# Performance work log

Hardware: AMD Instinct MI355X
Metric: run time of the kernel (lower is better)

Reference implementation:

```python
import jax, jax.numpy as jnp
import numpy as np

V = 64                 # |Sigma|
IN_DIM = V + 2         # Sigma + '(' + ')'
OUT_DIM = V + 1        # Sigma + <del>/<end>
H = 512
B = 256
SX = 34                # max proto length 32 + 2 boundaries
SY = 34
BIG_NEG = -1000000000.0


def _one_hot_seq(key, S, batch):
    # '(' at pos 0, L random symbols, ')' at pos L+1, zero padding after
    kl, ks = jax.random.split(key)
    lengths = jax.random.randint(kl, (batch,), 4, S - 1)        # L in [4, S-2]
    syms = jax.random.randint(ks, (S, batch), 0, V)
    pos = jnp.arange(S)[:, None]
    tok = jnp.where(pos == 0, V, jnp.where(pos == lengths[None, :] + 1, V + 1, syms))
    oh = jax.nn.one_hot(tok, IN_DIM, dtype=jnp.float32)
    valid = (pos <= lengths[None, :] + 1).astype(jnp.float32)
    return oh * valid[:, :, None]


def setup_inputs() -> dict:
    key = jax.random.key(0)
    ks = jax.random.split(key, 14)

    def p(k, shape, scale):
        return jax.random.uniform(k, shape, jnp.float32, -scale, scale)

    s = 1.0 / float(np.sqrt(H))
    s2 = 1.0 / float(np.sqrt(2 * H))
    return {
        "sources": _one_hot_seq(ks[0], SX, B),
        "targets": _one_hot_seq(ks[1], SY, B),
        # bidirectional prior LSTM (input IN_DIM -> hidden H, fwd + rev)
        "Wih_f": p(ks[2], (4 * H, IN_DIM), s), "Whh_f": p(ks[3], (4 * H, H), s), "b_f": p(ks[4], (4 * H,), s),
        "Wih_r": p(ks[5], (4 * H, IN_DIM), s), "Whh_r": p(ks[6], (4 * H, H), s), "b_r": p(ks[7], (4 * H,), s),
        # modern LSTM (input IN_DIM -> hidden 2H)
        "Wih_m": p(ks[8], (8 * H, IN_DIM), s2), "Whh_m": p(ks[9], (8 * H, 2 * H), s2), "b_m": p(ks[10], (8 * H,), s2),
        # heads: Linear(2H -> OUT_DIM) + LogSoftmax
        "W_sub": p(ks[11], (OUT_DIM, 2 * H), s2), "b_sub": jnp.zeros((OUT_DIM,), jnp.float32),
        "W_ins": p(ks[12], (OUT_DIM, 2 * H), s2), "b_ins": jnp.zeros((OUT_DIM,), jnp.float32),
    }


def _lstm(x, Wih, Whh, b, hid):
    # torch gate order: i, f, g, o
    bsz = x.shape[1]
    def step(carry, xt):
        h, c = carry
        g = xt @ Wih.T + h @ Whh.T + b
        i, f, gg, o = jnp.split(g, 4, axis=-1)
        c = jax.nn.sigmoid(f) * c + jax.nn.sigmoid(i) * jnp.tanh(gg)
        h = jax.nn.sigmoid(o) * jnp.tanh(c)
        return (h, c), h
    init = (jnp.zeros((bsz, hid), x.dtype), jnp.zeros((bsz, hid), x.dtype))
    _, hs = jax.lax.scan(step, init, x)
    return hs  # [S, B, hid]


def _forward(sources, targets, Wih_f, Whh_f, b_f, Wih_r, Whh_r, b_r,
             Wih_m, Whh_m, b_m, W_sub, b_sub, W_ins, b_ins):
    x_fwd = _lstm(sources, Wih_f, Whh_f, b_f, H)
    x_bwd = _lstm(sources[::-1], Wih_r, Whh_r, b_r, H)[::-1]
    x_emb = jnp.concatenate([x_fwd, x_bwd], axis=-1)   # [SX, B, 2H]
    y_emb = _lstm(targets, Wih_m, Whh_m, b_m, 2 * H)    # [SY, B, 2H]

    # head(x_emb[i] + y_emb[j]) decomposes since Linear is affine
    def pair_logprobs(W, bb):
        lx = jnp.einsum('ibh,oh->ibo', x_emb, W)              # [SX, B, O]
        ly = jnp.einsum('jbh,oh->jbo', y_emb, W) + bb         # [SY, B, O]
        return jax.nn.log_softmax(lx[:, None] + ly[None, :], axis=-1)  # [SX, SY, B, O]

    sub_log = pair_logprobs(W_sub, b_sub)
    ins_log = pair_logprobs(W_ins, b_ins)

    # cell (i, j, b) is computed iff x[i] and y[j] are real (non-padding) one-hots, j <= max_cognat_length
    x_any = sources.sum(-1) > 0                                # [SX, B]
    y_any = targets.sum(-1) > 0                                # [SY, B]
    j_ok = jnp.arange(SY) < SY - 1
    valid = x_any[:, None, :] & (y_any & j_ok[:, None])[None, :, :]   # [SX, SY, B]

    end = jnp.where(valid, ins_log[..., V], BIG_NEG)           # insProbs[V_SIZE]
    dlt = jnp.where(valid, sub_log[..., V], BIG_NEG)           # subProbs[V_SIZE]

    y_next = jnp.pad(targets[1:], ((0, 1), (0, 0), (0, 0)))    # y[j+1], [SY, B, IN_DIM]
    ins_ok = valid & (y_next[..., IN_DIM - 1] == 0)[None]      # not bool(y[j+1, V_SIZE+1])
    ins_val = jnp.einsum('ijbv,jbv->ijb', ins_log[..., :V], y_next[..., :V])
    sub_val = jnp.einsum('ijbv,jbv->ijb', sub_log[..., :V], y_next[..., :V])

    # stacked cached probs: [ins, sub, end, del], each [SX, SY, B]
    return jnp.stack([
        jnp.where(ins_ok, ins_val, BIG_NEG),
        jnp.where(ins_ok, sub_val, BIG_NEG),
        end,
        dlt,
    ])


def reference(sources, targets, Wih_f, Whh_f, b_f, Wih_r, Whh_r, b_r,
              Wih_m, Whh_m, b_m, W_sub, b_sub, W_ins, b_ins):
    return _forward(sources, targets, Wih_f, Whh_f, b_f, Wih_r, Whh_r, b_r,
                    Wih_m, Whh_m, b_m, W_sub, b_sub, W_ins, b_ins)
```

## Files before the change

### kernel.cpp

```cpp
#include <hip/hip_runtime.h>

typedef __attribute__((ext_vector_type(4))) float f32x4;
typedef unsigned char u8;
typedef unsigned long long u64t;

#define BIG_NEG -1000000000.0f

static constexpr int B_  = 256;
static constexpr int SX_ = 34;
static constexpr int SY_ = 34;
static constexpr int IND = 66;
static constexpr int OP_ = 80;

__device__ __forceinline__ f32x4 mfma_fp8(long a, long b, f32x4 c) {
  return __builtin_amdgcn_mfma_f32_16x16x32_fp8_fp8(a, b, c, 0, 0, 0);
}
__device__ __forceinline__ float sigm(float x)  { return 1.0f / (1.0f + __expf(-x)); }
__device__ __forceinline__ float tanhx(float x) { return 2.0f * sigm(2.0f * x) - 1.0f; }
template <bool HI>
__device__ __forceinline__ unsigned pk2(float a, float b, unsigned old) {
  return __builtin_amdgcn_cvt_pk_fp8_f32(a, b, (int)old, HI);
}

__global__ __launch_bounds__(256) void prep_all(
    const float* __restrict__ src, const float* __restrict__ tgt,
    int* __restrict__ tok_x, int* __restrict__ tok_y,
    const float* __restrict__ Wsub, const float* __restrict__ Wins,
    u8* __restrict__ Wcat,
    const float* __restrict__ Wihf, const float* __restrict__ bf,
    const float* __restrict__ Wihr, const float* __restrict__ br,
    const float* __restrict__ Wihm, const float* __restrict__ bm,
    float* __restrict__ Ef, float* __restrict__ Er, float* __restrict__ Em,
    const float* __restrict__ Whf, const float* __restrict__ Whr,
    const float* __restrict__ Whm,
    u8* __restrict__ w8f, u8* __restrict__ w8r, u8* __restrict__ w8m) {
  __shared__ float tile[64 * 67];
  const int blk = blockIdx.x;
  const int tid = threadIdx.x;

  if (blk < 68) {
    int idx = blk * 256 + tid;
    const int half = SX_ * B_;
    const float* base = (idx < half) ? src : tgt;
    int* outp         = (idx < half) ? tok_x : tok_y;
    int k = (idx < half) ? idx : idx - half;
    const float* p = base + (size_t)k * IND;
    int tok = -1;
    for (int v = 0; v < IND; ++v) if (p[v] > 0.5f) tok = v;
    outp[k] = tok;
  } else if (blk < 228) {
    int widx = (blk - 68) * 256 + tid;
    int row = widx >> 8;
    int wc  = widx & 255;
    int srow = row < 80 ? row : row - 80;
    const float* W = row < 80 ? Wsub : Wins;
    float f0 = 0.f, f1 = 0.f, f2 = 0.f, f3 = 0.f;
    if (srow < 65) {
      const float* p = W + (size_t)srow * 1024 + wc * 4;
      f0 = p[0]; f1 = p[1]; f2 = p[2]; f3 = p[3];
    }
    unsigned w = pk2<false>(f0, f1, 0);
    w = pk2<true>(f2, f3, w);
    ((unsigned*)Wcat)[widx] = w;
  } else if (blk < 356) {
    int tb = blk - 228;
    const float* W; const float* bias; float* E; int H4; int n0;
    if (tb < 32)      { W = Wihf; bias = bf; E = Ef; H4 = 2048; n0 = tb * 64; }
    else if (tb < 64) { W = Wihr; bias = br; E = Er; H4 = 2048; n0 = (tb - 32) * 64; }
    else              { W = Wihm; bias = bm; E = Em; H4 = 4096; n0 = (tb - 64) * 64; }
    const float* s2 = W + (size_t)n0 * IND;
    for (int i = tid; i < 64 * IND; i += 256) {
      int n = i / IND, v = i - n * IND;
      tile[n * 67 + v] = s2[i];
    }
    __syncthreads();
    int lane = tid & 63, w2 = tid >> 6;
    float bl = bias[n0 + lane];
    for (int v = w2; v < 67; v += 4) {
      float val = (v < 66 ? tile[lane * 67 + v] : 0.f) + bl;
      E[(size_t)v * H4 + n0 + lane] = val;
    }
  } else {
    const int F4 = 2048 * 512 / 4;
    const int M4 = 4096 * 1024 / 4;
    int i = (blk - 356) * 256 + tid;
    int stride = 3072 * 256;
    for (; i < 2 * F4 + M4; i += stride) {
      const float* s3; unsigned* dst; int k;
      if (i < F4)          { s3 = Whf; dst = (unsigned*)w8f; k = i; }
      else if (i < 2 * F4) { s3 = Whr; dst = (unsigned*)w8r; k = i - F4; }
      else                 { s3 = Whm; dst = (unsigned*)w8m; k = i - 2 * F4; }
      float4 f = ((const float4*)s3)[k];
      unsigned w3 = pk2<false>(f.x, f.y, 0);
      w3 = pk2<true>(f.z, f.w, w3);
      dst[k] = w3;
    }
  }
}

template <int HH, int NS>
__device__ __forceinline__ void run_lstm(
    const u8* __restrict__ w8, const float* __restrict__ E,
    bool revr, u8* __restrict__ hall, int b0, int h0,
    unsigned* __restrict__ flags, int dom0, int myid,
    u8* __restrict__ alds, u8* __restrict__ hT, const u8* __restrict__ tok_small) {
  const int tid = threadIdx.x;
  const int lane = tid & 63, w = tid >> 6;
  const int lo = lane & 15, q = lane >> 4;
  constexpr int AST = HH + 8;
  constexpr int U8C = HH / 8;
  constexpr int USH = (HH == 1024) ? 7 : 6;
  constexpr int NI  = (32 * U8C) / 256;
  constexpr int NK  = HH / 32;
  const int hh = lo & 7;
  const bool hi = (lo >= 8);
  const int hu_e = h0 + w * 8 + hh;

  long breg0[NK], breg1[NK];
  {
    const u8* brow0 = w8 + (size_t)((lo >> 3) * HH + hu_e) * HH + q * 8;
    const u8* brow1 = w8 + (size_t)((2 + (lo >> 3)) * HH + hu_e) * HH + q * 8;
#pragma unroll
    for (int kk = 0; kk < NK; ++kk) {
      breg0[kk] = *(const long*)(brow0 + kk * 32);
      breg1[kk] = *(const long*)(brow1 + kk * 32);
    }
  }
  float creg[4] = {0.f, 0.f, 0.f, 0.f};

  for (int t = 0; t < 34; ++t) {
    f32x4 acc[2][2];
#pragma unroll
    for (int mt = 0; mt < 2; ++mt) {
      acc[mt][0] = (f32x4){0.f, 0.f, 0.f, 0.f};
      acc[mt][1] = (f32x4){0.f, 0.f, 0.f, 0.f};
    }

    if (t > 0) {
      const u8* hsrc = hall + (size_t)t * (256 * HH);
      u64t tmp[NI];
#pragma unroll
      for (int ii = 0; ii < NI; ++ii) {
        int idx = tid + ii * 256;
        tmp[ii] = __hip_atomic_load(
            (const u64t*)(hsrc + (size_t)(b0 + (idx >> USH)) * HH + (idx & (U8C - 1)) * 8),
            __ATOMIC_RELAXED, __HIP_MEMORY_SCOPE_AGENT);
      }
#pragma unroll
      for (int ii = 0; ii < NI; ++ii) {
        int idx = tid + ii * 256;
        *(u64t*)&alds[(idx >> USH) * AST + (idx & (U8C - 1)) * 8] = tmp[ii];
      }
      __syncthreads();

      const u8* a0p = alds + lo * AST + q * 8;
      const u8* a1p = alds + (16 + lo) * AST + q * 8;
#pragma unroll
      for (int kk = 0; kk < NK; ++kk) {
        long a0 = *(const long*)(a0p + kk * 32);
        long a1 = *(const long*)(a1p + kk * 32);
        acc[0][0] = mfma_fp8(a0, breg0[kk], acc[0][0]);
        acc[0][1] = mfma_fp8(a0, breg1[kk], acc[0][1]);
        acc[1][0] = mfma_fp8(a1, breg0[kk], acc[1][0]);
        acc[1][1] = mfma_fp8(a1, breg1[kk], acc[1][1]);
      }
    }

    int tpos = revr ? 33 - t : t;
    const u8* tkp = tok_small + tpos * 32;
#pragma unroll
    for (int mt = 0; mt < 2; ++mt) {
      f32x4 t0 = acc[mt][0], t1 = acc[mt][1];
      f32x4 p0, p1;
#pragma unroll
      for (int c2 = 0; c2 < 4; ++c2) {
        p0[c2] = __shfl_xor(t0[c2], 8, 64);
        p1[c2] = __shfl_xor(t1[c2], 8, 64);
      }
#pragma unroll
      for (int rr = 0; rr < 2; ++rr) {
        int r = (hi ? 2 : 0) + rr;
        float iv = hi ? p0[r] : t0[r];
        float fv = hi ? t0[r] : p0[r];
        float gv = hi ? p1[r] : t1[r];
        float ov = hi ? t1[r] : p1[r];
        int m = mt * 16 + q * 4 + r;
        int v = tkp[m];
        const float* e = E + (size_t)v * (4 * HH) + hu_e;
        iv += e[0]; fv += e[HH]; gv += e[2 * HH]; ov += e[3 * HH];
        float cold = creg[mt * 2 + rr];
        float cn = sigm(fv) * cold + sigm(iv) * tanhx(gv);
        float hn = sigm(ov) * tanhx(cn);
        creg[mt * 2 + rr] = cn;
        hT[m * 32 + w * 8 + hh] = (u8)(pk2<false>(hn, hn, 0) & 0xffu);
      }
    }
    __syncthreads();

    {
      int m = tid >> 3, cc = tid & 7;
      unsigned val = *(const unsigned*)&hT[m * 32 + cc * 4];
      u8* hdst = hall + (size_t)(t + 1) * (256 * HH);
      __hip_atomic_store((unsigned*)(hdst + (size_t)(b0 + m) * HH + h0 + cc * 4),
                         val, __ATOMIC_RELAXED, __HIP_MEMORY_SCOPE_AGENT);
    }

    if (t < 33) {
      __asm__ volatile("s_waitcnt vmcnt(0)" ::: "memory");
      __syncthreads();
      unsigned tgt = (unsigned)(t + 1);
      if (tid == 0)
        __hip_atomic_store(&flags[(dom0 + myid) * 32], tgt,
                           __ATOMIC_RELAXED, __HIP_MEMORY_SCOPE_AGENT);
      if (tid < NS) {
        int spin = 0;
        for (;;) {
          unsigned v = __hip_atomic_load(&flags[(dom0 + tid) * 32],
                                         __ATOMIC_RELAXED, __HIP_MEMORY_SCOPE_AGENT);
          if (__ballot(v < tgt) == 0) break;
          __builtin_amdgcn_s_sleep(1);
          if (++spin > (1 << 17)) break;
        }
      }
      __syncthreads();
    }
  }
}

__global__ __launch_bounds__(256, 2) void lstm_persist(
    const int* __restrict__ tok_x, const int* __restrict__ tok_y,
    const float* __restrict__ E_f, const u8* __restrict__ w8_f,
    const float* __restrict__ E_r, const u8* __restrict__ w8_r,
    const float* __restrict__ E_m, const u8* __restrict__ w8_m,
    u8* __restrict__ fwd_all, u8* __restrict__ rev_all, u8* __restrict__ y_all,
    unsigned* __restrict__ flags) {
  __shared__ u8 alds[32 * 1032];
  __shared__ u8 hT[32 * 32];
  __shared__ u8 tok_small[34 * 32];

  const int b = blockIdx.x;
  int role, c, s;
  if (b < 256)      { role = 2; c = b >> 5; s = b & 31; }
  else if (b < 384) { int l = b - 256; role = 0; c = l >> 4; s = l & 15; }
  else              { int l = b - 384; role = 1; c = l >> 4; s = l & 15; }

  const float* E  = role == 0 ? E_f  : role == 1 ? E_r  : E_m;
  const u8*    w8 = role == 0 ? w8_f : role == 1 ? w8_r : w8_m;
  u8* hall        = role == 0 ? fwd_all : role == 1 ? rev_all : y_all;
  const int* tokg = (role == 2) ? tok_y : tok_x;
  const int b0 = c * 32;
  const int h0 = s * 32;
  const int dom0 = (role == 2) ? c * 32 : (role == 0) ? 256 + c * 16 : 384 + c * 16;

  for (int i = threadIdx.x; i < 34 * 32; i += 256) {
    int t2 = i >> 5, m = i & 31;
    int tk = tokg[t2 * 256 + b0 + m];
    tok_small[i] = (u8)(tk < 0 ? 66 : tk);
  }
  __syncthreads();

  if (role == 2)
    run_lstm<1024, 32>(w8, E, false, hall, b0, h0, flags, dom0, s, alds, hT, tok_small);
  else
    run_lstm<512, 16>(w8, E, role == 1, hall, b0, h0, flags, dom0, s, alds, hT, tok_small);
}

__global__ __launch_bounds__(256, 1) void head_kernel(
    const u8* __restrict__ fwd_all, const u8* __restrict__ rev_all,
    const u8* __restrict__ y_all, const u8* __restrict__ Wcat,
    const float* __restrict__ b_sub, const float* __restrict__ b_ins,
    float* __restrict__ lx_sub, float* __restrict__ lx_ins,
    float* __restrict__ ly_sub, float* __restrict__ ly_ins) {
  __shared__ u8 wq[160 * 264];
  const int lane = threadIdx.x & 63, wave = threadIdx.x >> 6;
  const int lo = lane & 15, q = lane >> 4;
  int blk = blockIdx.x;
  bool yside = (blk >= 136);
  int mb = yside ? blk - 136 : blk;
  int ij = mb >> 2;
  int bbase = (mb & 3) * 64;

  f32x4 acc[10];
#pragma unroll
  for (int nn = 0; nn < 10; ++nn) acc[nn] = (f32x4){0.f,0.f,0.f,0.f};

  for (int qk = 0; qk < 4; ++qk) {
    long aA[8];
    {
      int row = bbase + wave * 16 + lo;
      const u8* ab;
      if (yside)
        ab = y_all + ((size_t)(ij + 1) * 256 + row) * 1024 + qk * 256 + q * 8;
      else if (qk < 2)
        ab = fwd_all + ((size_t)(ij + 1) * 256 + row) * 512 + qk * 256 + q * 8;
      else
        ab = rev_all + ((size_t)(34 - ij) * 256 + row) * 512 + (qk - 2) * 256 + q * 8;
#pragma unroll
      for (int ki = 0; ki < 8; ++ki) aA[ki] = *(const long*)(ab + ki * 32);
    }

    for (int c8 = threadIdx.x; c8 < 160 * 32; c8 += 256) {
      int row = c8 >> 5, col = (c8 & 31) << 3;
      *(long*)&wq[row * 264 + col] =
          *(const long*)&Wcat[(size_t)row * 1024 + qk * 256 + col];
    }
    __syncthreads();

#pragma unroll
    for (int ki = 0; ki < 8; ++ki) {
#pragma unroll
      for (int nn = 0; nn < 10; ++nn) {
        long bf = *(const long*)&wq[(nn * 16 + lo) * 264 + ki * 32 + q * 8];
        acc[nn] = mfma_fp8(aA[ki], bf, acc[nn]);
      }
    }
    __syncthreads();
  }

#pragma unroll
  for (int nn = 0; nn < 10; ++nn) {
    bool is_sub = (nn < 5);
    int n = (is_sub ? nn : nn - 5) * 16 + lo;
    float bias = 0.0f;
    if (yside && n < 65) bias = is_sub ? b_sub[n] : b_ins[n];
    float* dst = yside ? (is_sub ? ly_sub : ly_ins) : (is_sub ? lx_sub : lx_ins);
#pragma unroll
    for (int r = 0; r < 4; ++r) {
      int b = bbase + wave * 16 + q * 4 + r;
      dst[((size_t)ij * 256 + b) * OP_ + n] = acc[nn][r] + bias;
    }
  }
}

__device__ __forceinline__ void lse_one(const float4* __restrict__ X,
                                        const float* __restrict__ py, int sym,
                                        float& logZ, float& v64, float& vs) {
  float v[68];
  const float4* py4 = (const float4*)py;
#pragma unroll
  for (int q = 0; q < 17; ++q) {
    float4 yb = py4[q];
    v[4 * q + 0] = X[q].x + yb.x;
    v[4 * q + 1] = X[q].y + yb.y;
    v[4 * q + 2] = X[q].z + yb.z;
    v[4 * q + 3] = X[q].w + yb.w;
  }
  float m = v[0];
#pragma unroll
  for (int o = 1; o < 65; ++o) m = fmaxf(m, v[o]);
  float s = 0.0f, vsl = 0.0f;
#pragma unroll
  for (int o = 0; o < 65; ++o) {
    s += __expf(v[o] - m);
    if (o < 64) vsl = (o == sym) ? v[o] : vsl;
  }
  logZ = m + __logf(s);
  v64 = v[64];
  vs = vsl;
}

__global__ __launch_bounds__(256, 1) void pair_kernel(
    const int* __restrict__ tok_x, const int* __restrict__ tok_y,
    const float* __restrict__ lx_sub, const float* __restrict__ lx_ins,
    const float* __restrict__ ly_sub, const float* __restrict__ ly_ins,
    float* __restrict__ out) {
  const int hsel = blockIdx.x >= 136;
  const int rem = hsel ? blockIdx.x - 136 : blockIdx.x;
  const int i = rem >> 2;
  const int bc = rem & 3;
  const int jq = threadIdx.x >> 6;
  const int bl = threadIdx.x & 63;
  const int b = bc * 64 + bl;
  const size_t CH = (size_t)SX_ * SY_ * B_;
  const float* lx = hsel ? lx_ins : lx_sub;
  const float* ly = hsel ? ly_ins : ly_sub;
  float* outA = out + (hsel ? 0 : CH);
  float* outB = out + (hsel ? 2 * CH : 3 * CH);

  float4 X[17];
  {
    const float4* ps = (const float4*)(lx + ((size_t)i * 256 + b) * OP_);
#pragma unroll
    for (int q = 0; q < 17; ++q) X[q] = ps[q];
  }
  int tx = tok_x[i * 256 + b];

  for (int j = jq; j < 34; j += 4) {
    size_t obase = ((size_t)i * SY_ + j) * 256 + b;
    bool dead = (j == SY_ - 1) || (tx < 0);
    if (!dead) {
      int ty = tok_y[j * 256 + b];
      if (ty < 0) dead = true;
    }
    if (dead) {
      outA[obase] = BIG_NEG;
      outB[obase] = BIG_NEG;
      continue;
    }
    int tn = tok_y[(j + 1) * 256 + b];
    bool ins_ok = (tn != 65);
    int sym = (tn >= 0 && tn < 64) ? tn : -1;

    float logZ, v64, vs;
    lse_one(X, ly + ((size_t)j * 256 + b) * OP_, sym, logZ, v64, vs);
    float valB = v64 - logZ;
    float valA = (sym >= 0) ? (vs - logZ) : 0.0f;
    outA[obase] = ins_ok ? valA : BIG_NEG;
    outB[obase] = valB;
  }
}

extern "C" void kernel_launch(void* const* d_in, const int* in_sizes, int n_in,
                              void* d_out, int out_size, void* d_ws, size_t ws_size,
                              hipStream_t stream) {
  const float* sources = (const float*)d_in[0];
  const float* targets = (const float*)d_in[1];
  const float* Wih_f = (const float*)d_in[2];
  const float* Whh_f = (const float*)d_in[3];
  const float* b_f   = (const float*)d_in[4];
  const float* Wih_r = (const float*)d_in[5];
  const float* Whh_r = (const float*)d_in[6];
  const float* b_r   = (const float*)d_in[7];
  const float* Wih_m = (const float*)d_in[8];
  const float* Whh_m = (const float*)d_in[9];
  const float* b_m   = (const float*)d_in[10];
  const float* W_sub = (const float*)d_in[11];
  const float* b_sub = (const float*)d_in[12];
  const float* W_ins = (const float*)d_in[13];
  const float* b_ins = (const float*)d_in[14];
  float* out = (float*)d_out;

  char* w = (char*)d_ws;
  constexpr size_t FLAG_SZ = 512 * 32 * 4;
  constexpr size_t TOK_SZ  = (size_t)SX_ * B_ * 4;
  constexpr size_t WCAT_SZ = (size_t)160 * 1024;
  constexpr size_t W8F_SZ  = (size_t)2048 * 512;
  constexpr size_t W8M_SZ  = (size_t)4096 * 1024;
  constexpr size_t EF_SZ   = (size_t)67 * 2048 * 4;
  constexpr size_t EM_SZ   = (size_t)67 * 4096 * 4;
  constexpr size_t LX_SZ   = (size_t)SX_ * B_ * OP_ * 4;
  constexpr size_t HF_SZ   = (size_t)35 * B_ * 512;
  constexpr size_t HM_SZ   = (size_t)35 * B_ * 1024;

  size_t off = 0;
  unsigned* flags = (unsigned*)(w + off); off += FLAG_SZ;
  int*  tok_x   = (int*)(w + off);  off += TOK_SZ;
  int*  tok_y   = (int*)(w + off);  off += TOK_SZ;
  off = (off + 255) & ~(size_t)255;
  u8*   Wcat    = (u8*)(w + off);   off += WCAT_SZ;
  u8*   w8_f    = (u8*)(w + off);   off += W8F_SZ;
  u8*   w8_r    = (u8*)(w + off);   off += W8F_SZ;
  u8*   w8_m    = (u8*)(w + off);   off += W8M_SZ;
  float* E_f    = (float*)(w + off); off += EF_SZ;
  float* E_r    = (float*)(w + off); off += EF_SZ;
  float* E_m    = (float*)(w + off); off += EM_SZ;
  float* lx_sub = (float*)(w + off); off += LX_SZ;
  float* lx_ins = (float*)(w + off); off += LX_SZ;
  float* ly_sub = (float*)(w + off); off += LX_SZ;
  float* ly_ins = (float*)(w + off); off += LX_SZ;
  u8* fwd_all   = (u8*)(w + off);   off += HF_SZ;
  u8* rev_all   = (u8*)(w + off);   off += HF_SZ;
  u8* y_all     = (u8*)(w + off);   off += HM_SZ;
  (void)ws_size; (void)in_sizes; (void)n_in; (void)out_size;

  (void)hipMemsetAsync(flags, 0, FLAG_SZ, stream);

  prep_all<<<3428, 256, 0, stream>>>(
      sources, targets, tok_x, tok_y,
      W_sub, W_ins, Wcat,
      Wih_f, b_f, Wih_r, b_r, Wih_m, b_m, E_f, E_r, E_m,
      Whh_f, Whh_r, Whh_m, w8_f, w8_r, w8_m);

  lstm_persist<<<512, 256, 0, stream>>>(
      tok_x, tok_y,
      E_f, w8_f,
      E_r, w8_r,
      E_m, w8_m,
      fwd_all, rev_all, y_all, flags);

  head_kernel<<<272, 256, 0, stream>>>(fwd_all, rev_all, y_all, Wcat,
                                       b_sub, b_ins, lx_sub, lx_ins, ly_sub, ly_ins);

  pair_kernel<<<272, 256, 0, stream>>>(tok_x, tok_y, lx_sub, lx_ins,
                                       ly_sub, ly_ins, out);
}
```

Baseline: 338.6 us.

## Split LSTM batch tile into two half-tiles with separate flags to overlap sync

The persistent LSTM kernel now processes each 32-row batch tile as two 16-row halves, each with its own completion flag domain. The second half's hidden-state loads and input-embedding gathers are issued while the first half's results are published, and separate waves wait on each half's flags. The aim is to shorten the critical path of the per-timestep cross-block barrier by letting dependent blocks start on half A before half B is done. In exchange there are more __syncthreads per step, a larger flag array, and half-width MFMA work per phase.

```diff
diff --git a/kernel.cpp b/kernel.cpp
--- a/kernel.cpp
+++ b/kernel.cpp
@@ -98,11 +98,36 @@
   }
 }
 
+__device__ __forceinline__ void lstm_epi(
+    f32x4 t0, f32x4 t1, const float (&e)[4][2], float (&creg)[2],
+    int r0, bool hi, int q, int w, int hh, u8* __restrict__ hT) {
+  f32x4 p0, p1;
+#pragma unroll
+  for (int c2 = 0; c2 < 4; ++c2) {
+    p0[c2] = __shfl_xor(t0[c2], 8, 64);
+    p1[c2] = __shfl_xor(t1[c2], 8, 64);
+  }
+#pragma unroll
+  for (int rr = 0; rr < 2; ++rr) {
+    int r = r0 + rr;
+    float iv = (hi ? p0[r] : t0[r]) + e[0][rr];
+    float fv = (hi ? t0[r] : p0[r]) + e[1][rr];
+    float gv = (hi ? p1[r] : t1[r]) + e[2][rr];
+    float ov = (hi ? t1[r] : p1[r]) + e[3][rr];
+    int m = q * 4 + r;
+    float cold = creg[rr];
+    float cn = sigm(fv) * cold + sigm(iv) * tanhx(gv);
+    float hn = sigm(ov) * tanhx(cn);
+    creg[rr] = cn;
+    hT[m * 32 + w * 8 + hh] = (u8)(pk2<false>(hn, hn, 0) & 0xffu);
+  }
+}
+
 template <int HH, int NS>
-__device__ __forceinline__ void run_lstm(
+__device__ __forceinline__ void run_lstm2(
     const u8* __restrict__ w8, const float* __restrict__ E,
     bool revr, u8* __restrict__ hall, int b0, int h0,
-    unsigned* __restrict__ flags, int dom0, int myid,
+    unsigned* __restrict__ flags, int fA, int fB, int myid,
     u8* __restrict__ alds, u8* __restrict__ hT, const u8* __restrict__ tok_small) {
   const int tid = threadIdx.x;
   const int lane = tid & 63, w = tid >> 6;
@@ -110,11 +135,12 @@
   constexpr int AST = HH + 8;
   constexpr int U8C = HH / 8;
   constexpr int USH = (HH == 1024) ? 7 : 6;
-  constexpr int NI  = (32 * U8C) / 256;
+  constexpr int NI  = (16 * U8C) / 256;
   constexpr int NK  = HH / 32;
   const int hh = lo & 7;
   const bool hi = (lo >= 8);
   const int hu_e = h0 + w * 8 + hh;
+  const int r0 = hi ? 2 : 0;
 
   long breg0[NK], breg1[NK];
   {
@@ -126,104 +152,136 @@
       breg1[kk] = *(const long*)(brow1 + kk * 32);
     }
   }
-  float creg[4] = {0.f, 0.f, 0.f, 0.f};
+  float cregA[2] = {0.f, 0.f};
+  float cregB[2] = {0.f, 0.f};
 
   for (int t = 0; t < 34; ++t) {
-    f32x4 acc[2][2];
-#pragma unroll
-    for (int mt = 0; mt < 2; ++mt) {
-      acc[mt][0] = (f32x4){0.f, 0.f, 0.f, 0.f};
-      acc[mt][1] = (f32x4){0.f, 0.f, 0.f, 0.f};
-    }
-
+    const int tpos = revr ? 33 - t : t;
+    const u8* tk_base = tok_small + tpos * 32;
+    const u8* hsrc = hall + (size_t)t * (256 * HH);
+    u8* hdst = hall + (size_t)(t + 1) * (256 * HH);
+
+    float eA[4][2];
     if (t > 0) {
-      const u8* hsrc = hall + (size_t)t * (256 * HH);
-      u64t tmp[NI];
+      u64t tmpA[NI];
 #pragma unroll
       for (int ii = 0; ii < NI; ++ii) {
         int idx = tid + ii * 256;
-        tmp[ii] = __hip_atomic_load(
+        tmpA[ii] = __hip_atomic_load(
             (const u64t*)(hsrc + (size_t)(b0 + (idx >> USH)) * HH + (idx & (U8C - 1)) * 8),
             __ATOMIC_RELAXED, __HIP_MEMORY_SCOPE_AGENT);
       }
 #pragma unroll
+      for (int rr = 0; rr < 2; ++rr) {
+        int v = tk_base[q * 4 + r0 + rr];
+        const float* e = E + (size_t)v * (4 * HH) + hu_e;
+        eA[0][rr] = e[0]; eA[1][rr] = e[HH]; eA[2][rr] = e[2 * HH]; eA[3][rr] = e[3 * HH];
+      }
+#pragma unroll
       for (int ii = 0; ii < NI; ++ii) {
         int idx = tid + ii * 256;
-        *(u64t*)&alds[(idx >> USH) * AST + (idx & (U8C - 1)) * 8] = tmp[ii];
+        *(u64t*)&alds[(idx >> USH) * AST + (idx & (U8C - 1)) * 8] = tmpA[ii];
       }
       __syncthreads();
-
-      const u8* a0p = alds + lo * AST + q * 8;
-      const u8* a1p = alds + (16 + lo) * AST + q * 8;
+    } else {
+#pragma unroll
+      for (int rr = 0; rr < 2; ++rr) {
+        int v = tk_base[q * 4 + r0 + rr];
+        const float* e = E + (size_t)v * (4 * HH) + hu_e;
+        eA[0][rr] = e[0]; eA[1][rr] = e[HH]; eA[2][rr] = e[2 * HH]; eA[3][rr] = e[3 * HH];
+      }
+    }
+
+    f32x4 accA0 = (f32x4){0.f, 0.f, 0.f, 0.f};
+    f32x4 accA1 = (f32x4){0.f, 0.f, 0.f, 0.f};
+    if (t > 0) {
+      const u8* ap = alds + lo * AST + q * 8;
 #pragma unroll
       for (int kk = 0; kk < NK; ++kk) {
-        long a0 = *(const long*)(a0p + kk * 32);
-        long a1 = *(const long*)(a1p + kk * 32);
-        acc[0][0] = mfma_fp8(a0, breg0[kk], acc[0][0]);
-        acc[0][1] = mfma_fp8(a0, breg1[kk], acc[0][1]);
-        acc[1][0] = mfma_fp8(a1, breg0[kk], acc[1][0]);
-        acc[1][1] = mfma_fp8(a1, breg1[kk], acc[1][1]);
-      }
-    }
-
-    int tpos = revr ? 33 - t : t;
-    const u8* tkp = tok_small + tpos * 32;
-#pragma unroll
-    for (int mt = 0; mt < 2; ++mt) {
-      f32x4 t0 = acc[mt][0], t1 = acc[mt][1];
-      f32x4 p0, p1;
-#pragma unroll
-      for (int c2 = 0; c2 < 4; ++c2) {
-        p0[c2] = __shfl_xor(t0[c2], 8, 64);
-        p1[c2] = __shfl_xor(t1[c2], 8, 64);
-      }
-#pragma unroll
-      for (int rr = 0; rr < 2; ++rr) {
-        int r = (hi ? 2 : 0) + rr;
-        float iv = hi ? p0[r] : t0[r];
-        float fv = hi ? t0[r] : p0[r];
-        float gv = hi ? p1[r] : t1[r];
-        float ov = hi ? t1[r] : p1[r];
-        int m = mt * 16 + q * 4 + r;
-        int v = tkp[m];
-        const float* e = E + (size_t)v * (4 * HH) + hu_e;
-        iv += e[0]; fv += e[HH]; gv += e[2 * HH]; ov += e[3 * HH];
-        float cold = creg[mt * 2 + rr];
-        float cn = sigm(fv) * cold + sigm(iv) * tanhx(gv);
-        float hn = sigm(ov) * tanhx(cn);
-        creg[mt * 2 + rr] = cn;
-        hT[m * 32 + w * 8 + hh] = (u8)(pk2<false>(hn, hn, 0) & 0xffu);
-      }
-    }
-    __syncthreads();
-
-    {
-      int m = tid >> 3, cc = tid & 7;
-      unsigned val = *(const unsigned*)&hT[m * 32 + cc * 4];
-      u8* hdst = hall + (size_t)(t + 1) * (256 * HH);
-      __hip_atomic_store((unsigned*)(hdst + (size_t)(b0 + m) * HH + h0 + cc * 4),
+        long av = *(const long*)(ap + kk * 32);
+        accA0 = mfma_fp8(av, breg0[kk], accA0);
+        accA1 = mfma_fp8(av, breg1[kk], accA1);
+      }
+    }
+    lstm_epi(accA0, accA1, eA, cregA, r0, hi, q, w, hh, hT);
+    __syncthreads();
+
+    float eB[4][2];
+    u64t tmpB[NI];
+    if (t > 0) {
+#pragma unroll
+      for (int ii = 0; ii < NI; ++ii) {
+        int idx = tid + ii * 256;
+        tmpB[ii] = __hip_atomic_load(
+            (const u64t*)(hsrc + (size_t)(b0 + 16 + (idx >> USH)) * HH + (idx & (U8C - 1)) * 8),
+            __ATOMIC_RELAXED, __HIP_MEMORY_SCOPE_AGENT);
+      }
+    }
+    if (w == 0) {
+      int m = lane >> 2, c8 = lane & 3;
+      u64t val = *(const u64t*)&hT[m * 32 + c8 * 8];
+      __hip_atomic_store((u64t*)(hdst + (size_t)(b0 + m) * HH + h0 + c8 * 8),
                          val, __ATOMIC_RELAXED, __HIP_MEMORY_SCOPE_AGENT);
-    }
-
-    if (t < 33) {
       __asm__ volatile("s_waitcnt vmcnt(0)" ::: "memory");
-      __syncthreads();
-      unsigned tgt = (unsigned)(t + 1);
-      if (tid == 0)
-        __hip_atomic_store(&flags[(dom0 + myid) * 32], tgt,
+      if (lane == 0 && t < 33)
+        __hip_atomic_store(&flags[(fA + myid) * 32], (unsigned)(t + 1),
                            __ATOMIC_RELAXED, __HIP_MEMORY_SCOPE_AGENT);
-      if (tid < NS) {
+    }
+#pragma unroll
+    for (int rr = 0; rr < 2; ++rr) {
+      int v = tk_base[16 + q * 4 + r0 + rr];
+      const float* e = E + (size_t)v * (4 * HH) + hu_e;
+      eB[0][rr] = e[0]; eB[1][rr] = e[HH]; eB[2][rr] = e[2 * HH]; eB[3][rr] = e[3 * HH];
+    }
+    if (t > 0) {
+#pragma unroll
+      for (int ii = 0; ii < NI; ++ii) {
+        int idx = tid + ii * 256;
+        *(u64t*)&alds[(16 + (idx >> USH)) * AST + (idx & (U8C - 1)) * 8] = tmpB[ii];
+      }
+    }
+    __syncthreads();
+
+    f32x4 accB0 = (f32x4){0.f, 0.f, 0.f, 0.f};
+    f32x4 accB1 = (f32x4){0.f, 0.f, 0.f, 0.f};
+    if (t > 0) {
+      const u8* ap = alds + (16 + lo) * AST + q * 8;
+#pragma unroll
+      for (int kk = 0; kk < NK; ++kk) {
+        long av = *(const long*)(ap + kk * 32);
+        accB0 = mfma_fp8(av, breg0[kk], accB0);
+        accB1 = mfma_fp8(av, breg1[kk], accB1);
+      }
+    }
+    lstm_epi(accB0, accB1, eB, cregB, r0, hi, q, w, hh, hT);
+    __syncthreads();
+
+    if (w == 0) {
+      int m = lane >> 2, c8 = lane & 3;
+      u64t val = *(const u64t*)&hT[m * 32 + c8 * 8];
+      __hip_atomic_store((u64t*)(hdst + (size_t)(b0 + 16 + m) * HH + h0 + c8 * 8),
+                         val, __ATOMIC_RELAXED, __HIP_MEMORY_SCOPE_AGENT);
+      if (t < 33) {
+        __asm__ volatile("s_waitcnt vmcnt(0)" ::: "memory");
+        if (lane == 0)
+          __hip_atomic_store(&flags[(fB + myid) * 32], (unsigned)(t + 1),
+                             __ATOMIC_RELAXED, __HIP_MEMORY_SCOPE_AGENT);
+      }
+    } else if ((w == 2 || w == 3) && t < 33) {
+      const int base = (w == 2) ? fA : fB;
+      const unsigned tgt = (unsigned)(t + 1);
+      if (lane < NS) {
         int spin = 0;
         for (;;) {
-          unsigned v = __hip_atomic_load(&flags[(dom0 + tid) * 32],
+          unsigned v = __hip_atomic_load(&flags[(base + lane) * 32],
                                          __ATOMIC_RELAXED, __HIP_MEMORY_SCOPE_AGENT);
           if (__ballot(v < tgt) == 0) break;
           __builtin_amdgcn_s_sleep(1);
           if (++spin > (1 << 17)) break;
         }
       }
-      __syncthreads();
-    }
+    }
+    __syncthreads();
   }
 }
 
@@ -234,8 +292,8 @@
     const float* __restrict__ E_m, const u8* __restrict__ w8_m,
     u8* __restrict__ fwd_all, u8* __restrict__ rev_all, u8* __restrict__ y_all,
     unsigned* __restrict__ flags) {
-  __shared__ u8 alds[32 * 1032];
-  __shared__ u8 hT[32 * 32];
+  __shared__ u8 alds[32 * 1032] __attribute__((aligned(16)));
+  __shared__ u8 hT[16 * 32] __attribute__((aligned(16)));
   __shared__ u8 tok_small[34 * 32];
 
   const int b = blockIdx.x;
@@ -250,7 +308,10 @@
   const int* tokg = (role == 2) ? tok_y : tok_x;
   const int b0 = c * 32;
   const int h0 = s * 32;
-  const int dom0 = (role == 2) ? c * 32 : (role == 0) ? 256 + c * 16 : 384 + c * 16;
+  int fA, fB;
+  if (role == 2)      { fA = c * 64;        fB = fA + 32; }
+  else if (role == 0) { fA = 512 + c * 32;  fB = fA + 16; }
+  else                { fA = 768 + c * 32;  fB = fA + 16; }
 
   for (int i = threadIdx.x; i < 34 * 32; i += 256) {
     int t2 = i >> 5, m = i & 31;
@@ -260,9 +321,9 @@
   __syncthreads();
 
   if (role == 2)
-    run_lstm<1024, 32>(w8, E, false, hall, b0, h0, flags, dom0, s, alds, hT, tok_small);
+    run_lstm2<1024, 32>(w8, E, false, hall, b0, h0, flags, fA, fB, s, alds, hT, tok_small);
   else
-    run_lstm<512, 16>(w8, E, role == 1, hall, b0, h0, flags, dom0, s, alds, hT, tok_small);
+    run_lstm2<512, 16>(w8, E, role == 1, hall, b0, h0, flags, fA, fB, s, alds, hT, tok_small);
 }
 
 __global__ __launch_bounds__(256, 1) void head_kernel(
@@ -431,7 +492,7 @@
   float* out = (float*)d_out;
 
   char* w = (char*)d_ws;
-  constexpr size_t FLAG_SZ = 512 * 32 * 4;
+  constexpr size_t FLAG_SZ = 1024 * 32 * 4;
   constexpr size_t TOK_SZ  = (size_t)SX_ * B_ * 4;
   constexpr size_t WCAT_SZ = (size_t)160 * 1024;
   constexpr size_t W8F_SZ  = (size_t)2048 * 512;
```

New measurement: 378.2 us. +11.7%, slower.

## Replace LSTM flag barrier with poison-value polling on hidden-state data

Applied to the files above, without the earlier changes.

Removes the per-timestep flag store and spin barrier between the blocks of each LSTM domain. Each block instead pre-fills the hidden-state history buffers with a 0x7F poison pattern and re-reads the previous step's h until no 32-bit word still holds that pattern. This turns the global barrier into a point-to-point data dependency. The input-embedding gate contributions are now loaded before the wait, so their latency overlaps it. The cost is a much larger memset of all hidden-state buffers at launch, plus repeated global re-reads of the h tile while spinning.

```diff
diff --git a/kernel.cpp b/kernel.cpp
--- a/kernel.cpp
+++ b/kernel.cpp
@@ -98,11 +98,10 @@
   }
 }
 
-template <int HH, int NS>
+template <int HH>
 __device__ __forceinline__ void run_lstm(
     const u8* __restrict__ w8, const float* __restrict__ E,
     bool revr, u8* __restrict__ hall, int b0, int h0,
-    unsigned* __restrict__ flags, int dom0, int myid,
     u8* __restrict__ alds, u8* __restrict__ hT, const u8* __restrict__ tok_small) {
   const int tid = threadIdx.x;
   const int lane = tid & 63, w = tid >> 6;
@@ -115,6 +114,7 @@
   const int hh = lo & 7;
   const bool hi = (lo >= 8);
   const int hu_e = h0 + w * 8 + hh;
+  const unsigned POI = 0x7F7F7F7Fu;
 
   long breg0[NK], breg1[NK];
   {
@@ -129,6 +129,23 @@
   float creg[4] = {0.f, 0.f, 0.f, 0.f};
 
   for (int t = 0; t < 34; ++t) {
+    const int tpos = revr ? 33 - t : t;
+    const u8* tkp = tok_small + tpos * 32;
+
+    float ev[2][4][2];
+#pragma unroll
+    for (int mt = 0; mt < 2; ++mt)
+#pragma unroll
+      for (int rr = 0; rr < 2; ++rr) {
+        int r = (hi ? 2 : 0) + rr;
+        int v = tkp[mt * 16 + q * 4 + r];
+        const float* e = E + (size_t)v * (4 * HH) + hu_e;
+        ev[mt][0][rr] = e[0];
+        ev[mt][1][rr] = e[HH];
+        ev[mt][2][rr] = e[2 * HH];
+        ev[mt][3][rr] = e[3 * HH];
+      }
+
     f32x4 acc[2][2];
 #pragma unroll
     for (int mt = 0; mt < 2; ++mt) {
@@ -139,12 +156,19 @@
     if (t > 0) {
       const u8* hsrc = hall + (size_t)t * (256 * HH);
       u64t tmp[NI];
-#pragma unroll
-      for (int ii = 0; ii < NI; ++ii) {
-        int idx = tid + ii * 256;
-        tmp[ii] = __hip_atomic_load(
-            (const u64t*)(hsrc + (size_t)(b0 + (idx >> USH)) * HH + (idx & (U8C - 1)) * 8),
-            __ATOMIC_RELAXED, __HIP_MEMORY_SCOPE_AGENT);
+      int spin = 0;
+      for (;;) {
+        int bad = 0;
+#pragma unroll
+        for (int ii = 0; ii < NI; ++ii) {
+          int idx = tid + ii * 256;
+          tmp[ii] = __hip_atomic_load(
+              (const u64t*)(hsrc + (size_t)(b0 + (idx >> USH)) * HH + (idx & (U8C - 1)) * 8),
+              __ATOMIC_RELAXED, __HIP_MEMORY_SCOPE_AGENT);
+          bad |= ((unsigned)tmp[ii] == POI) | ((unsigned)(tmp[ii] >> 32) == POI);
+        }
+        if (!__syncthreads_or(bad)) break;
+        if (++spin > (1 << 15)) break;
       }
 #pragma unroll
       for (int ii = 0; ii < NI; ++ii) {
@@ -166,8 +190,6 @@
       }
     }
 
-    int tpos = revr ? 33 - t : t;
-    const u8* tkp = tok_small + tpos * 32;
 #pragma unroll
     for (int mt = 0; mt < 2; ++mt) {
       f32x4 t0 = acc[mt][0], t1 = acc[mt][1];
@@ -180,14 +202,11 @@
 #pragma unroll
       for (int rr = 0; rr < 2; ++rr) {
         int r = (hi ? 2 : 0) + rr;
-        float iv = hi ? p0[r] : t0[r];
-        float fv = hi ? t0[r] : p0[r];
-        float gv = hi ? p1[r] : t1[r];
-        float ov = hi ? t1[r] : p1[r];
+        float iv = (hi ? p0[r] : t0[r]) + ev[mt][0][rr];
+        float fv = (hi ? t0[r] : p0[r]) + ev[mt][1][rr];
+        float gv = (hi ? p1[r] : t1[r]) + ev[mt][2][rr];
+        float ov = (hi ? t1[r] : p1[r]) + ev[mt][3][rr];
         int m = mt * 16 + q * 4 + r;
-        int v = tkp[m];
-        const float* e = E + (size_t)v * (4 * HH) + hu_e;
-        iv += e[0]; fv += e[HH]; gv += e[2 * HH]; ov += e[3 * HH];
         float cold = creg[mt * 2 + rr];
         float cn = sigm(fv) * cold + sigm(iv) * tanhx(gv);
         float hn = sigm(ov) * tanhx(cn);
@@ -204,26 +223,6 @@
       __hip_atomic_store((unsigned*)(hdst + (size_t)(b0 + m) * HH + h0 + cc * 4),
                          val, __ATOMIC_RELAXED, __HIP_MEMORY_SCOPE_AGENT);
     }
-
-    if (t < 33) {
-      __asm__ volatile("s_waitcnt vmcnt(0)" ::: "memory");
-      __syncthreads();
-      unsigned tgt = (unsigned)(t + 1);
-      if (tid == 0)
-        __hip_atomic_store(&flags[(dom0 + myid) * 32], tgt,
-                           __ATOMIC_RELAXED, __HIP_MEMORY_SCOPE_AGENT);
-      if (tid < NS) {
-        int spin = 0;
-        for (;;) {
-          unsigned v = __hip_atomic_load(&flags[(dom0 + tid) * 32],
-                                         __ATOMIC_RELAXED, __HIP_MEMORY_SCOPE_AGENT);
-          if (__ballot(v < tgt) == 0) break;
-          __builtin_amdgcn_s_sleep(1);
-          if (++spin > (1 << 17)) break;
-        }
-      }
-      __syncthreads();
-    }
   }
 }
 
@@ -232,10 +231,9 @@
     const float* __restrict__ E_f, const u8* __restrict__ w8_f,
     const float* __restrict__ E_r, const u8* __restrict__ w8_r,
     const float* __restrict__ E_m, const u8* __restrict__ w8_m,
-    u8* __restrict__ fwd_all, u8* __restrict__ rev_all, u8* __restrict__ y_all,
-    unsigned* __restrict__ flags) {
-  __shared__ u8 alds[32 * 1032];
-  __shared__ u8 hT[32 * 32];
+    u8* __restrict__ fwd_all, u8* __restrict__ rev_all, u8* __restrict__ y_all) {
+  __shared__ u8 alds[32 * 1032] __attribute__((aligned(16)));
+  __shared__ u8 hT[32 * 32] __attribute__((aligned(16)));
   __shared__ u8 tok_small[34 * 32];
 
   const int b = blockIdx.x;
@@ -250,7 +248,6 @@
   const int* tokg = (role == 2) ? tok_y : tok_x;
   const int b0 = c * 32;
   const int h0 = s * 32;
-  const int dom0 = (role == 2) ? c * 32 : (role == 0) ? 256 + c * 16 : 384 + c * 16;
 
   for (int i = threadIdx.x; i < 34 * 32; i += 256) {
     int t2 = i >> 5, m = i & 31;
@@ -260,9 +257,9 @@
   __syncthreads();
 
   if (role == 2)
-    run_lstm<1024, 32>(w8, E, false, hall, b0, h0, flags, dom0, s, alds, hT, tok_small);
+    run_lstm<1024>(w8, E, false, hall, b0, h0, alds, hT, tok_small);
   else
-    run_lstm<512, 16>(w8, E, role == 1, hall, b0, h0, flags, dom0, s, alds, hT, tok_small);
+    run_lstm<512>(w8, E, role == 1, hall, b0, h0, alds, hT, tok_small);
 }
 
 __global__ __launch_bounds__(256, 1) void head_kernel(
@@ -431,7 +428,6 @@
   float* out = (float*)d_out;
 
   char* w = (char*)d_ws;
-  constexpr size_t FLAG_SZ = 512 * 32 * 4;
   constexpr size_t TOK_SZ  = (size_t)SX_ * B_ * 4;
   constexpr size_t WCAT_SZ = (size_t)160 * 1024;
   constexpr size_t W8F_SZ  = (size_t)2048 * 512;
@@ -443,7 +439,6 @@
   constexpr size_t HM_SZ   = (size_t)35 * B_ * 1024;
 
   size_t off = 0;
-  unsigned* flags = (unsigned*)(w + off); off += FLAG_SZ;
   int*  tok_x   = (int*)(w + off);  off += TOK_SZ;
   int*  tok_y   = (int*)(w + off);  off += TOK_SZ;
   off = (off + 255) & ~(size_t)255;
@@ -463,7 +458,7 @@
   u8* y_all     = (u8*)(w + off);   off += HM_SZ;
   (void)ws_size; (void)in_sizes; (void)n_in; (void)out_size;
 
-  (void)hipMemsetAsync(flags, 0, FLAG_SZ, stream);
+  (void)hipMemsetAsync(fwd_all, 0x7F, HF_SZ * 2 + HM_SZ, stream);
 
   prep_all<<<3428, 256, 0, stream>>>(
       sources, targets, tok_x, tok_y,
@@ -476,7 +471,7 @@
       E_f, w8_f,
       E_r, w8_r,
       E_m, w8_m,
-      fwd_all, rev_all, y_all, flags);
+      fwd_all, rev_all, y_all);
 
   head_kernel<<<272, 256, 0, stream>>>(fwd_all, rev_all, y_all, Wcat,
                                        b_sub, b_ins, lx_sub, lx_ins, ly_sub, ly_ins);
```

Measured after the change: 398.5 us. 1.18x slower.
